# Kernel tuning notes

Measured on AMD Instinct MI355X. Metric: run time of the kernel, lower is better.

## Reference

```python
import jax, jax.numpy as jnp
import numpy as np

N_NODES = 50000
C = 128
E = 800000
B = 4096
NEG = 5
NUM_LAYERS = 3


def setup_inputs() -> dict:
    key = jax.random.key(0)
    ks = jax.random.split(key, 8)
    edge_index = jax.random.randint(ks[0], (2, E), 0, N_NODES, dtype=jnp.int64)
    edge_weight = jax.random.uniform(ks[1], (E,), dtype=jnp.float32)
    n_id = jax.random.randint(ks[2], ((2 + NEG) * B,), 0, N_NODES, dtype=jnp.int64)
    x = jnp.zeros((1,), jnp.float32)  # ignored by forward (overwritten by id_embed)
    id_embed = jax.random.normal(ks[3], (N_NODES, C), jnp.float32) * 0.1
    w1 = jax.random.normal(ks[4], (2 * C, C), jnp.float32) * (1.0 / np.sqrt(2 * C))
    b1 = jnp.zeros((C,), jnp.float32)
    w2 = jax.random.normal(ks[5], (C, 1), jnp.float32) * (1.0 / np.sqrt(C))
    b2 = jnp.zeros((1,), jnp.float32)
    return {"x": x, "edge_index": edge_index, "edge_weight": edge_weight,
            "n_id": n_id, "neg_sample_num": NEG, "id_embed": id_embed,
            "w1": w1, "b1": b1, "w2": w2, "b2": b2}


def reference(x, edge_index, edge_weight, n_id, neg_sample_num, id_embed, w1, b1, w2, b2):
    n_nodes = id_embed.shape[0]
    row, col = edge_index[0], edge_index[1]
    # symmetric GCN normalization (LGCConv)
    deg = jax.ops.segment_sum(jnp.ones_like(row, dtype=id_embed.dtype), row,
                              num_segments=n_nodes)
    dinv = jnp.where(deg > 0, jax.lax.rsqrt(jnp.maximum(deg, 1e-12)), 0.0)
    norm = (dinv[row] * dinv[col])[:, None]  # [E,1]
    h = id_embed
    final = id_embed
    for _ in range(NUM_LAYERS):
        h = jax.ops.segment_sum(norm * h[col], row, num_segments=n_nodes)
        final = final + h
    final = final / (NUM_LAYERS + 1)
    # split n_id into (out, pos, neg) index groups
    b = n_id.shape[0] // (2 + neg_sample_num)
    out = final[n_id[:b]]
    pos = final[n_id[b:2 * b]]
    neg = final[n_id[2 * b:]]
    tiled_out = jnp.repeat(out, neg_sample_num, axis=0)  # [b*neg, C]

    def pred_head(z):  # Linear -> LeakyReLU(0.2) -> (Dropout eval=identity) -> Linear
        z = jax.nn.leaky_relu(z @ w1 + b1, negative_slope=0.2)
        return z @ w2 + b2

    pos_logit = pred_head(jnp.concatenate([out, pos], axis=-1))
    neg_logits = pred_head(jnp.concatenate([tiled_out, neg], axis=-1))
    return pos_logit, neg_logits
```

## Files before the change

### kernel.cpp

```cpp
#include <hip/hip_runtime.h>
#include <hip/hip_bf16.h>

#define C 128
#define NBKT 128
#define BCAP 8192

typedef __bf16 bf16x8 __attribute__((ext_vector_type(8)));
typedef float floatx4 __attribute__((ext_vector_type(4)));

__device__ __forceinline__ unsigned short f2bf(float f) {
    unsigned u = __float_as_uint(f);
    unsigned r = (u + 0x7FFFu + ((u >> 16) & 1u)) >> 16;
    return (unsigned short)r;
}
__device__ __forceinline__ float bflo(unsigned v) { return __uint_as_float(v << 16); }
__device__ __forceinline__ float bfhi(unsigned v) { return __uint_as_float(v & 0xFFFF0000u); }
__device__ __forceinline__ unsigned packbf(float lo, float hi) {
    return (unsigned)f2bf(lo) | ((unsigned)f2bf(hi) << 16);
}

__device__ __forceinline__ int g_idx(const void* p, long long i, int is64) {
    if (is64) return (int)((const long long*)p)[i];
    return ((const int*)p)[i];
}
__device__ __forceinline__ float g_flt(const void* p, long long i, int isf32) {
    if (isf32) return ((const float*)p)[i];
    return __uint_as_float(((unsigned)((const unsigned short*)p)[i]) << 16);
}

__global__ void k_detect(const void* edge, const void* nid, const void* emb, int* flags,
                         unsigned* g0, unsigned* g1, unsigned* g2, int* bucketcnt, int N) {
    int t = threadIdx.x;
    int buf = t >> 6, w = t & 63;
    size_t o = (size_t)N * 64 + w;
    if (buf == 0) g0[o] = 0;
    else if (buf == 1) g1[o] = 0;
    else g2[o] = 0;
    if (t < NBKT) bucketcnt[t] = 0;
    if (t < 64) {
        const unsigned* wrd = (const unsigned*)edge;
        const unsigned* nw = (const unsigned*)nid;
        int predA = (t < 32) ? (wrd[2 * t + 1] == 0u) : 1;
        int predB = (t < 32) ? (nw[2 * t + 1] == 0u) : 1;
        const unsigned short* h = (const unsigned short*)emb;
        int ex = (h[2 * t] >> 7) & 0xFF;
        int plaus = (ex >= 0x6C && ex <= 0x7F) ? 1 : 0;
        unsigned long long mA = __ballot(predA);
        unsigned long long mB = __ballot(predB);
        unsigned long long mP = __ballot(plaus);
        if (t == 0) {
            flags[0] = (mA == ~0ull) ? 1 : 0;
            flags[1] = (mB == ~0ull) ? 1 : 0;
            flags[2] = (__popcll(mP) < 32) ? 1 : 0;
        }
    }
}

__global__ void k_bucketA(const void* edge, int E, int rpb, const int* flags,
                          unsigned* __restrict__ bucketbuf, int* __restrict__ bucketcnt) {
    __shared__ int lcnt[NBKT];
    __shared__ int lbase[NBKT];
    int t = threadIdx.x;
    int is64 = flags[0];
    const int PER = 8;
    int chunkSz = blockDim.x * PER;
    long long stride = (long long)gridDim.x * chunkSz;
    for (long long base = (long long)blockIdx.x * chunkSz; base < E; base += stride) {
        if (t < NBKT) lcnt[t] = 0;
        __syncthreads();
        int bkt[PER], rank[PER];
        unsigned enc[PER];
        long long e0 = base + (long long)t * PER;
        int rr[PER], cc[PER];
        if (e0 + PER <= E) {
            if (is64) {
                const long long* pr = (const long long*)edge + e0;
                const long long* pc = (const long long*)edge + E + e0;
#pragma unroll
                for (int j = 0; j < PER; j += 2) {
                    longlong2 vr = *(const longlong2*)(pr + j);
                    longlong2 vc = *(const longlong2*)(pc + j);
                    rr[j] = (int)vr.x; rr[j + 1] = (int)vr.y;
                    cc[j] = (int)vc.x; cc[j + 1] = (int)vc.y;
                }
            } else {
                const int* pr = (const int*)edge + e0;
                const int* pc = (const int*)edge + E + e0;
#pragma unroll
                for (int j = 0; j < PER; j += 4) {
                    int4 vr = *(const int4*)(pr + j);
                    int4 vc = *(const int4*)(pc + j);
                    rr[j] = vr.x; rr[j + 1] = vr.y; rr[j + 2] = vr.z; rr[j + 3] = vr.w;
                    cc[j] = vc.x; cc[j + 1] = vc.y; cc[j + 2] = vc.z; cc[j + 3] = vc.w;
                }
            }
#pragma unroll
            for (int j = 0; j < PER; ++j) {
                int b = rr[j] / rpb;
                bkt[j] = b;
                enc[j] = ((unsigned)(rr[j] - b * rpb) << 16) | (unsigned)(cc[j] & 0xFFFF);
                rank[j] = atomicAdd(&lcnt[b], 1);
            }
        } else {
#pragma unroll
            for (int j = 0; j < PER; ++j) {
                long long e = e0 + j;
                if (e < E) {
                    int r = g_idx(edge, e, is64);
                    int c = g_idx(edge, (long long)E + e, is64);
                    int b = r / rpb;
                    bkt[j] = b;
                    enc[j] = ((unsigned)(r - b * rpb) << 16) | (unsigned)(c & 0xFFFF);
                    rank[j] = atomicAdd(&lcnt[b], 1);
                } else bkt[j] = -1;
            }
        }
        __syncthreads();
        if (t < NBKT) lbase[t] = atomicAdd(&bucketcnt[t], lcnt[t]);
        __syncthreads();
#pragma unroll
        for (int j = 0; j < PER; ++j) {
            if (bkt[j] >= 0) {
                int pos = lbase[bkt[j]] + rank[j];
                if (pos < BCAP)
                    bucketbuf[(size_t)bkt[j] * BCAP + pos] = enc[j];
            }
        }
    }
}

__global__ __launch_bounds__(512) void k_bsort(
        const unsigned* __restrict__ bucketbuf, const int* __restrict__ bucketcnt,
        int* __restrict__ rowptr, float* __restrict__ dinv, float* __restrict__ di2,
        float* __restrict__ rdinv, unsigned short* __restrict__ cols16, int N, int rpb) {
    __shared__ int hist[512];
    int b = blockIdx.x;
    int t = threadIdx.x;
    int base = 0, cnt = 0, total = 0;
    for (int i = 0; i < NBKT; ++i) {
        int v = bucketcnt[i];
        if (v > BCAP) v = BCAP;
        if (i < b) base += v;
        if (i == b) cnt = v;
        total += v;
    }
    int r0 = b * rpb;
    int rows = N - r0;
    if (rows > rpb) rows = rpb;
    if (rows < 0) rows = 0;

    hist[t] = 0;
    __syncthreads();
    const unsigned* buf = bucketbuf + (size_t)b * BCAP;
    for (int i = t; i < cnt; i += 512) atomicAdd(&hist[buf[i] >> 16], 1);
    __syncthreads();
    int v = hist[t];
    __syncthreads();
    for (int off = 1; off < 512; off <<= 1) {
        int x = (t >= off) ? hist[t - off] : 0;
        __syncthreads();
        hist[t] += x;
        __syncthreads();
    }
    int excl = hist[t] - v;
    if (t < rows) {
        int r = r0 + t;
        rowptr[r] = base + excl;
        float fd = (float)v;
        float dv = (v > 0) ? rsqrtf(fd) : 0.0f;
        dinv[r] = dv;
        di2[r] = dv * dv;
        rdinv[r] = (v > 0) ? sqrtf(fd) : 0.0f;
    }
    if (b == NBKT - 1 && t == 0) rowptr[N] = total;
    __syncthreads();
    hist[t] = base + excl;
    __syncthreads();
    for (int i = t; i < cnt; i += 512) {
        unsigned u = buf[i];
        int pos = atomicAdd(&hist[u >> 16], 1);
        cols16[pos] = (unsigned short)(u & 0xFFFF);
    }
}

__global__ void k_initprep(const void* emb, const float* __restrict__ dinv,
                           unsigned* __restrict__ h0, unsigned* __restrict__ g0, int n2,
                           const void* w1, const void* b1, const void* w2, const void* b2,
                           unsigned short* __restrict__ w1t, float* __restrict__ b1f,
                           float* __restrict__ w2f, float* __restrict__ b2f, const int* flags) {
    int i = blockIdx.x * blockDim.x + threadIdx.x;
    int f32 = flags[2];
    if (i < n2) {
        float lo = g_flt(emb, 2LL * i, f32);
        float hi = g_flt(emb, 2LL * i + 1, f32);
        h0[i] = packbf(lo, hi);
        float dv = dinv[i >> 6];
        g0[i] = packbf(lo * dv, hi * dv);
    }
    if (i < 256 * 128) {
        int k = i >> 7, n = i & 127;
        w1t[n * 256 + k] = f2bf(g_flt(w1, i, f32));
    }
    if (i < 128) {
        b1f[i] = g_flt(b1, i, f32);
        w2f[i] = g_flt(w2, i, f32);
    }
    if (i == 0) b2f[0] = g_flt(b2, 0, f32);
}

__global__ void k_layer(const int* __restrict__ rowptr, const unsigned short* __restrict__ cols16,
                        const uint4* __restrict__ gin, uint4* __restrict__ gout,
                        const float* __restrict__ di2, int N) {
    int node = blockIdx.x * (blockDim.x >> 6) + (threadIdx.x >> 6);
    if (node >= N) return;
    int lane = threadIdx.x & 63;
    int quad = lane >> 4, l16 = lane & 15;
    int p = rowptr[node];
    int end = rowptr[node + 1];
    float a0 = 0.f, a1 = 0.f, a2 = 0.f, a3 = 0.f;
    float a4 = 0.f, a5 = 0.f, a6 = 0.f, a7 = 0.f;
    for (int base = p; base < end; base += 16) {
        int i0 = base + (quad << 2);
        int c0 = cols16[i0];
        int c1 = cols16[i0 + 1];
        int c2 = cols16[i0 + 2];
        int c3 = cols16[i0 + 3];
        c0 = (i0 < end) ? c0 : N;
        c1 = (i0 + 1 < end) ? c1 : N;
        c2 = (i0 + 2 < end) ? c2 : N;
        c3 = (i0 + 3 < end) ? c3 : N;
        uint4 v0 = gin[(size_t)c0 * 16 + l16];
        uint4 v1 = gin[(size_t)c1 * 16 + l16];
        uint4 v2 = gin[(size_t)c2 * 16 + l16];
        uint4 v3 = gin[(size_t)c3 * 16 + l16];
        a0 += (bflo(v0.x) + bflo(v1.x)) + (bflo(v2.x) + bflo(v3.x));
        a1 += (bfhi(v0.x) + bfhi(v1.x)) + (bfhi(v2.x) + bfhi(v3.x));
        a2 += (bflo(v0.y) + bflo(v1.y)) + (bflo(v2.y) + bflo(v3.y));
        a3 += (bfhi(v0.y) + bfhi(v1.y)) + (bfhi(v2.y) + bfhi(v3.y));
        a4 += (bflo(v0.z) + bflo(v1.z)) + (bflo(v2.z) + bflo(v3.z));
        a5 += (bfhi(v0.z) + bfhi(v1.z)) + (bfhi(v2.z) + bfhi(v3.z));
        a6 += (bflo(v0.w) + bflo(v1.w)) + (bflo(v2.w) + bflo(v3.w));
        a7 += (bfhi(v0.w) + bfhi(v1.w)) + (bfhi(v2.w) + bfhi(v3.w));
    }
    a0 += __shfl_xor(a0, 16, 64); a0 += __shfl_xor(a0, 32, 64);
    a1 += __shfl_xor(a1, 16, 64); a1 += __shfl_xor(a1, 32, 64);
    a2 += __shfl_xor(a2, 16, 64); a2 += __shfl_xor(a2, 32, 64);
    a3 += __shfl_xor(a3, 16, 64); a3 += __shfl_xor(a3, 32, 64);
    a4 += __shfl_xor(a4, 16, 64); a4 += __shfl_xor(a4, 32, 64);
    a5 += __shfl_xor(a5, 16, 64); a5 += __shfl_xor(a5, 32, 64);
    a6 += __shfl_xor(a6, 16, 64); a6 += __shfl_xor(a6, 32, 64);
    a7 += __shfl_xor(a7, 16, 64); a7 += __shfl_xor(a7, 32, 64);
    if (quad == 0) {
        float s = di2[node];
        uint4 o;
        o.x = packbf(a0 * s, a1 * s);
        o.y = packbf(a2 * s, a3 * s);
        o.z = packbf(a4 * s, a5 * s);
        o.w = packbf(a6 * s, a7 * s);
        gout[(size_t)node * 16 + l16] = o;
    }
}

__global__ void k_layer3(const int* __restrict__ rowptr, const unsigned short* __restrict__ cols16,
                         const uint4* __restrict__ gin , const uint4* __restrict__ h0,
                         const uint4* __restrict__ g1, uint4* __restrict__ fin,
                         const float* __restrict__ di2, const float* __restrict__ rdinv, int N) {
    int node = blockIdx.x * (blockDim.x >> 6) + (threadIdx.x >> 6);
    if (node >= N) return;
    int lane = threadIdx.x & 63;
    int quad = lane >> 4, l16 = lane & 15;
    int p = rowptr[node];
    int end = rowptr[node + 1];
    float a0 = 0.f, a1 = 0.f, a2 = 0.f, a3 = 0.f;
    float a4 = 0.f, a5 = 0.f, a6 = 0.f, a7 = 0.f;
    for (int base = p; base < end; base += 16) {
        int i0 = base + (quad << 2);
        int c0 = cols16[i0];
        int c1 = cols16[i0 + 1];
        int c2 = cols16[i0 + 2];
        int c3 = cols16[i0 + 3];
        c0 = (i0 < end) ? c0 : N;
        c1 = (i0 + 1 < end) ? c1 : N;
        c2 = (i0 + 2 < end) ? c2 : N;
        c3 = (i0 + 3 < end) ? c3 : N;
        uint4 v0 = gin[(size_t)c0 * 16 + l16];
        uint4 v1 = gin[(size_t)c1 * 16 + l16];
        uint4 v2 = gin[(size_t)c2 * 16 + l16];
        uint4 v3 = gin[(size_t)c3 * 16 + l16];
        a0 += (bflo(v0.x) + bflo(v1.x)) + (bflo(v2.x) + bflo(v3.x));
        a1 += (bfhi(v0.x) + bfhi(v1.x)) + (bfhi(v2.x) + bfhi(v3.x));
        a2 += (bflo(v0.y) + bflo(v1.y)) + (bflo(v2.y) + bflo(v3.y));
        a3 += (bfhi(v0.y) + bfhi(v1.y)) + (bfhi(v2.y) + bfhi(v3.y));
        a4 += (bflo(v0.z) + bflo(v1.z)) + (bflo(v2.z) + bflo(v3.z));
        a5 += (bfhi(v0.z) + bfhi(v1.z)) + (bfhi(v2.z) + bfhi(v3.z));
        a6 += (bflo(v0.w) + bflo(v1.w)) + (bflo(v2.w) + bflo(v3.w));
        a7 += (bfhi(v0.w) + bfhi(v1.w)) + (bfhi(v2.w) + bfhi(v3.w));
    }
    a0 += __shfl_xor(a0, 16, 64); a0 += __shfl_xor(a0, 32, 64);
    a1 += __shfl_xor(a1, 16, 64); a1 += __shfl_xor(a1, 32, 64);
    a2 += __shfl_xor(a2, 16, 64); a2 += __shfl_xor(a2, 32, 64);
    a3 += __shfl_xor(a3, 16, 64); a3 += __shfl_xor(a3, 32, 64);
    a4 += __shfl_xor(a4, 16, 64); a4 += __shfl_xor(a4, 32, 64);
    a5 += __shfl_xor(a5, 16, 64); a5 += __shfl_xor(a5, 32, 64);
    a6 += __shfl_xor(a6, 16, 64); a6 += __shfl_xor(a6, 32, 64);
    a7 += __shfl_xor(a7, 16, 64); a7 += __shfl_xor(a7, 32, 64);
    if (quad == 0) {
        float s = di2[node];
        float rd = rdinv[node];
        size_t ro = (size_t)node * 16 + l16;
        uint4 x0 = h0[ro];
        uint4 x1 = g1[ro];
        uint4 x2 = gin[ro];
        uint4 o;
        o.x = packbf(0.25f * (bflo(x0.x) + rd * (bflo(x1.x) + bflo(x2.x) + s * a0)),
                     0.25f * (bfhi(x0.x) + rd * (bfhi(x1.x) + bfhi(x2.x) + s * a1)));
        o.y = packbf(0.25f * (bflo(x0.y) + rd * (bflo(x1.y) + bflo(x2.y) + s * a2)),
                     0.25f * (bfhi(x0.y) + rd * (bfhi(x1.y) + bfhi(x2.y) + s * a3)));
        o.z = packbf(0.25f * (bflo(x0.z) + rd * (bflo(x1.z) + bflo(x2.z) + s * a4)),
                     0.25f * (bfhi(x0.z) + rd * (bfhi(x1.z) + bfhi(x2.z) + s * a5)));
        o.w = packbf(0.25f * (bflo(x0.w) + rd * (bflo(x1.w) + bflo(x2.w) + s * a6)),
                     0.25f * (bfhi(x0.w) + rd * (bfhi(x1.w) + bfhi(x2.w) + s * a7)));
        fin[ro] = o;
    }
}

__global__ void k_head(const unsigned* __restrict__ fin, const void* n_id,
                       const unsigned short* __restrict__ w1t,
                       const float* __restrict__ b1f, const float* __restrict__ w2f,
                       const float* __restrict__ b2f,
                       float* __restrict__ out, int B, int NEG, const int* flags) {
    __shared__ unsigned short z[64][264];
    int t = threadIdx.x;
    int id64 = flags[1];
    int mbase = blockIdx.x * 64;

    int tu = t & 63;
    int sel = t >> 6;
    int moff = sel >> 1, half = sel & 1;
    for (int m = 0; m < 64; m += 2) {
        int gm = mbase + m + moff;
        int r;
        if (gm < B) {
            r = half ? g_idx(n_id, B + gm, id64) : g_idx(n_id, gm, id64);
        } else {
            int j = gm - B;
            r = half ? g_idx(n_id, 2 * B + j, id64) : g_idx(n_id, j / NEG, id64);
        }
        ((unsigned*)&z[m + moff][0])[half * 64 + tu] = fin[(size_t)r * 64 + tu];
    }
    __syncthreads();

    int wave = t >> 6, lane = t & 63;
    int quad = lane >> 4, l16 = lane & 15;

    floatx4 acc[8] = {};
    bf16x8 a[8];
    const unsigned short* zrow = &z[wave * 16 + l16][0];
#pragma unroll
    for (int ks = 0; ks < 8; ++ks)
        a[ks] = *(const bf16x8*)(zrow + ks * 32 + quad * 8);

#pragma unroll
    for (int ks = 0; ks < 8; ++ks) {
#pragma unroll
        for (int nt = 0; nt < 8; ++nt) {
            bf16x8 b = *(const bf16x8*)(w1t + (nt * 16 + l16) * 256 + ks * 32 + quad * 8);
            acc[nt] = __builtin_amdgcn_mfma_f32_16x16x32_bf16(a[ks], b, acc[nt], 0, 0, 0);
        }
    }

    float s0 = 0.f, s1 = 0.f, s2 = 0.f, s3 = 0.f;
#pragma unroll
    for (int nt = 0; nt < 8; ++nt) {
        int col = nt * 16 + l16;
        float bb = b1f[col], ww = w2f[col];
        float v0 = acc[nt][0] + bb; v0 = (v0 > 0.f) ? v0 : 0.2f * v0; s0 += v0 * ww;
        float v1 = acc[nt][1] + bb; v1 = (v1 > 0.f) ? v1 : 0.2f * v1; s1 += v1 * ww;
        float v2 = acc[nt][2] + bb; v2 = (v2 > 0.f) ? v2 : 0.2f * v2; s2 += v2 * ww;
        float v3 = acc[nt][3] + bb; v3 = (v3 > 0.f) ? v3 : 0.2f * v3; s3 += v3 * ww;
    }
#pragma unroll
    for (int off = 1; off <= 8; off <<= 1) {
        s0 += __shfl_xor(s0, off, 64);
        s1 += __shfl_xor(s1, off, 64);
        s2 += __shfl_xor(s2, off, 64);
        s3 += __shfl_xor(s3, off, 64);
    }
    if (l16 == 0) {
        int rowbase = mbase + wave * 16 + quad * 4;
        float bb2 = b2f[0];
        out[rowbase + 0] = s0 + bb2;
        out[rowbase + 1] = s1 + bb2;
        out[rowbase + 2] = s2 + bb2;
        out[rowbase + 3] = s3 + bb2;
    }
}

extern "C" void kernel_launch(void* const* d_in, const int* in_sizes, int n_in,
                              void* d_out, int out_size, void* d_ws, size_t ws_size,
                              hipStream_t stream) {
    const void* edge_index = d_in[1];
    const void* n_id       = d_in[3];
    const void* id_embed   = d_in[5];
    const void* w1 = d_in[6];
    const void* b1 = d_in[7];
    const void* w2 = d_in[8];
    const void* b2 = d_in[9];
    float* out = (float*)d_out;

    const int E  = in_sizes[1] / 2;
    const int N  = in_sizes[5] / C;
    const int NEG = 5;
    const int B  = in_sizes[3] / (2 + NEG);
    const int n_out_rows = B + B * NEG;
    const int NB = (N + 1) * 64;
    const int rpb = (N + NBKT - 1) / NBKT;

    size_t off = 0;
    auto alloc = [&](size_t nf) {
        char* p = (char*)d_ws + off * 4;
        off += (nf + 255) & ~(size_t)255;
        return p;
    };
    int*   flags     = (int*)alloc(8);
    int*   bucketcnt = (int*)alloc(NBKT);
    float* dinv      = (float*)alloc(N);
    float* di2       = (float*)alloc(N);
    float* rdinv     = (float*)alloc(N);
    int*   rowptr    = (int*)alloc(N + 1);
    unsigned short* cols16 = (unsigned short*)alloc(((size_t)E + 16 + 1) / 2);
    unsigned* bucketbuf = (unsigned*)alloc((size_t)NBKT * BCAP);
    unsigned* h0     = (unsigned*)alloc(NB);
    unsigned* g0     = (unsigned*)alloc(NB);
    unsigned* g1     = (unsigned*)alloc(NB);
    unsigned* g2     = (unsigned*)alloc(NB);
    unsigned* fin    = (unsigned*)alloc((size_t)N * 64);
    unsigned short* w1t = (unsigned short*)alloc(256 * 128 / 2);
    float* b1f       = (float*)alloc(C);
    float* w2f       = (float*)alloc(C);
    float* b2f       = (float*)alloc(8);

    const int BS = 256;
    k_detect<<<1, 192, 0, stream>>>(edge_index, n_id, id_embed, flags, g0, g1, g2, bucketcnt, N);
    const int gridA = (E + BS * 8 - 1) / (BS * 8);
    k_bucketA<<<gridA, BS, 0, stream>>>(edge_index, E, rpb, flags, bucketbuf, bucketcnt);
    k_bsort<<<NBKT, 512, 0, stream>>>(bucketbuf, bucketcnt, rowptr, dinv, di2, rdinv,
                                      cols16, N, rpb);
    k_initprep<<<(N * 64 + BS - 1) / BS, BS, 0, stream>>>(
        id_embed, dinv, h0, g0, N * 64, w1, b1, w2, b2, w1t, b1f, w2f, b2f, flags);

    const int waves_per_block = BS / 64;
    const int layer_grid = (N + waves_per_block - 1) / waves_per_block;
    k_layer<<<layer_grid, BS, 0, stream>>>(rowptr, cols16, (const uint4*)g0, (uint4*)g1, di2, N);
    k_layer<<<layer_grid, BS, 0, stream>>>(rowptr, cols16, (const uint4*)g1, (uint4*)g2, di2, N);
    k_layer3<<<layer_grid, BS, 0, stream>>>(rowptr, cols16, (const uint4*)g2, (const uint4*)h0,
                                            (const uint4*)g1, (uint4*)fin, di2, rdinv, N);

    k_head<<<n_out_rows / 64, BS, 0, stream>>>(fin, n_id, w1t, b1f, w2f, b2f, out, B, NEG, flags);
}
```

Before: 249.4 us.

## Split node features into two channel slabs and assign eight lanes per node

The bf16 propagation buffers are stored as two separate 64-channel slabs. Each layer block works on one slab, with 8 lanes handling each node and walking its edges sequentially in steps of 4. This drops the cross-quad shuffle reduction and the predicated-off output lanes, and keeps each layer's random-gather working set at half the feature width, which should improve cache hit rates. The head gather now uses 16-byte loads. In exchange each node's edges are processed more serially, so load balance depends on the degree distribution, and adjacency reads happen twice, once per slab.

```diff
diff --git a/kernel.cpp b/kernel.cpp
--- a/kernel.cpp
+++ b/kernel.cpp
@@ -29,10 +29,11 @@
 }
 
 __global__ void k_detect(const void* edge, const void* nid, const void* emb, int* flags,
-                         unsigned* g0, unsigned* g1, unsigned* g2, int* bucketcnt, int N) {
+                         unsigned* g0, unsigned* g1, unsigned* g2, int* bucketcnt,
+                         int N, int SST) {
     int t = threadIdx.x;
     int buf = t >> 6, w = t & 63;
-    size_t o = (size_t)N * 64 + w;
+    size_t o = (size_t)(w >> 5) * SST + (size_t)N * 32 + (w & 31);
     if (buf == 0) g0[o] = 0;
     else if (buf == 1) g1[o] = 0;
     else g2[o] = 0;
@@ -184,7 +185,8 @@
 }
 
 __global__ void k_initprep(const void* emb, const float* __restrict__ dinv,
-                           unsigned* __restrict__ h0, unsigned* __restrict__ g0, int n2,
+                           unsigned* __restrict__ h0, unsigned* __restrict__ g0,
+                           int n2, int SST,
                            const void* w1, const void* b1, const void* w2, const void* b2,
                            unsigned short* __restrict__ w1t, float* __restrict__ b1f,
                            float* __restrict__ w2f, float* __restrict__ b2f, const int* flags) {
@@ -193,9 +195,11 @@
     if (i < n2) {
         float lo = g_flt(emb, 2LL * i, f32);
         float hi = g_flt(emb, 2LL * i + 1, f32);
-        h0[i] = packbf(lo, hi);
-        float dv = dinv[i >> 6];
-        g0[i] = packbf(lo * dv, hi * dv);
+        int n = i >> 6, w = i & 63;
+        size_t o = (size_t)(w >> 5) * SST + (size_t)n * 32 + (w & 31);
+        h0[o] = packbf(lo, hi);
+        float dv = dinv[n];
+        g0[o] = packbf(lo * dv, hi * dv);
     }
     if (i < 256 * 128) {
         int k = i >> 7, n = i & 127;
@@ -210,29 +214,28 @@
 
 __global__ void k_layer(const int* __restrict__ rowptr, const unsigned short* __restrict__ cols16,
                         const uint4* __restrict__ gin, uint4* __restrict__ gout,
-                        const float* __restrict__ di2, int N) {
-    int node = blockIdx.x * (blockDim.x >> 6) + (threadIdx.x >> 6);
+                        const float* __restrict__ di2, int N, int SSTU4) {
+    int slice = blockIdx.x & 1;
+    int node = (blockIdx.x >> 1) * 32 + (threadIdx.x >> 3);
     if (node >= N) return;
-    int lane = threadIdx.x & 63;
-    int quad = lane >> 4, l16 = lane & 15;
+    int l8 = threadIdx.x & 7;
+    const uint4* gs = gin + (size_t)slice * SSTU4;
     int p = rowptr[node];
     int end = rowptr[node + 1];
     float a0 = 0.f, a1 = 0.f, a2 = 0.f, a3 = 0.f;
     float a4 = 0.f, a5 = 0.f, a6 = 0.f, a7 = 0.f;
-    for (int base = p; base < end; base += 16) {
-        int i0 = base + (quad << 2);
-        int c0 = cols16[i0];
-        int c1 = cols16[i0 + 1];
-        int c2 = cols16[i0 + 2];
-        int c3 = cols16[i0 + 3];
-        c0 = (i0 < end) ? c0 : N;
-        c1 = (i0 + 1 < end) ? c1 : N;
-        c2 = (i0 + 2 < end) ? c2 : N;
-        c3 = (i0 + 3 < end) ? c3 : N;
-        uint4 v0 = gin[(size_t)c0 * 16 + l16];
-        uint4 v1 = gin[(size_t)c1 * 16 + l16];
-        uint4 v2 = gin[(size_t)c2 * 16 + l16];
-        uint4 v3 = gin[(size_t)c3 * 16 + l16];
+    for (int base = p; base < end; base += 4) {
+        int c0 = cols16[base];
+        int c1 = cols16[base + 1];
+        int c2 = cols16[base + 2];
+        int c3 = cols16[base + 3];
+        c1 = (base + 1 < end) ? c1 : N;
+        c2 = (base + 2 < end) ? c2 : N;
+        c3 = (base + 3 < end) ? c3 : N;
+        uint4 v0 = gs[(size_t)c0 * 8 + l8];
+        uint4 v1 = gs[(size_t)c1 * 8 + l8];
+        uint4 v2 = gs[(size_t)c2 * 8 + l8];
+        uint4 v3 = gs[(size_t)c3 * 8 + l8];
         a0 += (bflo(v0.x) + bflo(v1.x)) + (bflo(v2.x) + bflo(v3.x));
         a1 += (bfhi(v0.x) + bfhi(v1.x)) + (bfhi(v2.x) + bfhi(v3.x));
         a2 += (bflo(v0.y) + bflo(v1.y)) + (bflo(v2.y) + bflo(v3.y));
@@ -242,51 +245,42 @@
         a6 += (bflo(v0.w) + bflo(v1.w)) + (bflo(v2.w) + bflo(v3.w));
         a7 += (bfhi(v0.w) + bfhi(v1.w)) + (bfhi(v2.w) + bfhi(v3.w));
     }
-    a0 += __shfl_xor(a0, 16, 64); a0 += __shfl_xor(a0, 32, 64);
-    a1 += __shfl_xor(a1, 16, 64); a1 += __shfl_xor(a1, 32, 64);
-    a2 += __shfl_xor(a2, 16, 64); a2 += __shfl_xor(a2, 32, 64);
-    a3 += __shfl_xor(a3, 16, 64); a3 += __shfl_xor(a3, 32, 64);
-    a4 += __shfl_xor(a4, 16, 64); a4 += __shfl_xor(a4, 32, 64);
-    a5 += __shfl_xor(a5, 16, 64); a5 += __shfl_xor(a5, 32, 64);
-    a6 += __shfl_xor(a6, 16, 64); a6 += __shfl_xor(a6, 32, 64);
-    a7 += __shfl_xor(a7, 16, 64); a7 += __shfl_xor(a7, 32, 64);
-    if (quad == 0) {
-        float s = di2[node];
-        uint4 o;
-        o.x = packbf(a0 * s, a1 * s);
-        o.y = packbf(a2 * s, a3 * s);
-        o.z = packbf(a4 * s, a5 * s);
-        o.w = packbf(a6 * s, a7 * s);
-        gout[(size_t)node * 16 + l16] = o;
-    }
+    float s = di2[node];
+    uint4 o;
+    o.x = packbf(a0 * s, a1 * s);
+    o.y = packbf(a2 * s, a3 * s);
+    o.z = packbf(a4 * s, a5 * s);
+    o.w = packbf(a6 * s, a7 * s);
+    gout[(size_t)slice * SSTU4 + (size_t)node * 8 + l8] = o;
 }
 
 __global__ void k_layer3(const int* __restrict__ rowptr, const unsigned short* __restrict__ cols16,
                          const uint4* __restrict__ gin , const uint4* __restrict__ h0,
                          const uint4* __restrict__ g1, uint4* __restrict__ fin,
-                         const float* __restrict__ di2, const float* __restrict__ rdinv, int N) {
-    int node = blockIdx.x * (blockDim.x >> 6) + (threadIdx.x >> 6);
+                         const float* __restrict__ di2, const float* __restrict__ rdinv,
+                         int N, int SSTU4) {
+    int slice = blockIdx.x & 1;
+    int node = (blockIdx.x >> 1) * 32 + (threadIdx.x >> 3);
     if (node >= N) return;
-    int lane = threadIdx.x & 63;
-    int quad = lane >> 4, l16 = lane & 15;
+    int l8 = threadIdx.x & 7;
+    size_t sb = (size_t)slice * SSTU4;
+    const uint4* gs = gin + sb;
     int p = rowptr[node];
     int end = rowptr[node + 1];
     float a0 = 0.f, a1 = 0.f, a2 = 0.f, a3 = 0.f;
     float a4 = 0.f, a5 = 0.f, a6 = 0.f, a7 = 0.f;
-    for (int base = p; base < end; base += 16) {
-        int i0 = base + (quad << 2);
-        int c0 = cols16[i0];
-        int c1 = cols16[i0 + 1];
-        int c2 = cols16[i0 + 2];
-        int c3 = cols16[i0 + 3];
-        c0 = (i0 < end) ? c0 : N;
-        c1 = (i0 + 1 < end) ? c1 : N;
-        c2 = (i0 + 2 < end) ? c2 : N;
-        c3 = (i0 + 3 < end) ? c3 : N;
-        uint4 v0 = gin[(size_t)c0 * 16 + l16];
-        uint4 v1 = gin[(size_t)c1 * 16 + l16];
-        uint4 v2 = gin[(size_t)c2 * 16 + l16];
-        uint4 v3 = gin[(size_t)c3 * 16 + l16];
+    for (int base = p; base < end; base += 4) {
+        int c0 = cols16[base];
+        int c1 = cols16[base + 1];
+        int c2 = cols16[base + 2];
+        int c3 = cols16[base + 3];
+        c1 = (base + 1 < end) ? c1 : N;
+        c2 = (base + 2 < end) ? c2 : N;
+        c3 = (base + 3 < end) ? c3 : N;
+        uint4 v0 = gs[(size_t)c0 * 8 + l8];
+        uint4 v1 = gs[(size_t)c1 * 8 + l8];
+        uint4 v2 = gs[(size_t)c2 * 8 + l8];
+        uint4 v3 = gs[(size_t)c3 * 8 + l8];
         a0 += (bflo(v0.x) + bflo(v1.x)) + (bflo(v2.x) + bflo(v3.x));
         a1 += (bfhi(v0.x) + bfhi(v1.x)) + (bfhi(v2.x) + bfhi(v3.x));
         a2 += (bflo(v0.y) + bflo(v1.y)) + (bflo(v2.y) + bflo(v3.y));
@@ -296,35 +290,25 @@
         a6 += (bflo(v0.w) + bflo(v1.w)) + (bflo(v2.w) + bflo(v3.w));
         a7 += (bfhi(v0.w) + bfhi(v1.w)) + (bfhi(v2.w) + bfhi(v3.w));
     }
-    a0 += __shfl_xor(a0, 16, 64); a0 += __shfl_xor(a0, 32, 64);
-    a1 += __shfl_xor(a1, 16, 64); a1 += __shfl_xor(a1, 32, 64);
-    a2 += __shfl_xor(a2, 16, 64); a2 += __shfl_xor(a2, 32, 64);
-    a3 += __shfl_xor(a3, 16, 64); a3 += __shfl_xor(a3, 32, 64);
-    a4 += __shfl_xor(a4, 16, 64); a4 += __shfl_xor(a4, 32, 64);
-    a5 += __shfl_xor(a5, 16, 64); a5 += __shfl_xor(a5, 32, 64);
-    a6 += __shfl_xor(a6, 16, 64); a6 += __shfl_xor(a6, 32, 64);
-    a7 += __shfl_xor(a7, 16, 64); a7 += __shfl_xor(a7, 32, 64);
-    if (quad == 0) {
-        float s = di2[node];
-        float rd = rdinv[node];
-        size_t ro = (size_t)node * 16 + l16;
-        uint4 x0 = h0[ro];
-        uint4 x1 = g1[ro];
-        uint4 x2 = gin[ro];
-        uint4 o;
-        o.x = packbf(0.25f * (bflo(x0.x) + rd * (bflo(x1.x) + bflo(x2.x) + s * a0)),
-                     0.25f * (bfhi(x0.x) + rd * (bfhi(x1.x) + bfhi(x2.x) + s * a1)));
-        o.y = packbf(0.25f * (bflo(x0.y) + rd * (bflo(x1.y) + bflo(x2.y) + s * a2)),
-                     0.25f * (bfhi(x0.y) + rd * (bfhi(x1.y) + bfhi(x2.y) + s * a3)));
-        o.z = packbf(0.25f * (bflo(x0.z) + rd * (bflo(x1.z) + bflo(x2.z) + s * a4)),
-                     0.25f * (bfhi(x0.z) + rd * (bfhi(x1.z) + bfhi(x2.z) + s * a5)));
-        o.w = packbf(0.25f * (bflo(x0.w) + rd * (bflo(x1.w) + bflo(x2.w) + s * a6)),
-                     0.25f * (bfhi(x0.w) + rd * (bfhi(x1.w) + bfhi(x2.w) + s * a7)));
-        fin[ro] = o;
-    }
-}
-
-__global__ void k_head(const unsigned* __restrict__ fin, const void* n_id,
+    float s = di2[node];
+    float rd = rdinv[node];
+    size_t ro = (size_t)node * 8 + l8;
+    uint4 x0 = h0[sb + ro];
+    uint4 x1 = g1[sb + ro];
+    uint4 x2 = gs[ro];
+    uint4 o;
+    o.x = packbf(0.25f * (bflo(x0.x) + rd * (bflo(x1.x) + bflo(x2.x) + s * a0)),
+                 0.25f * (bfhi(x0.x) + rd * (bfhi(x1.x) + bfhi(x2.x) + s * a1)));
+    o.y = packbf(0.25f * (bflo(x0.y) + rd * (bflo(x1.y) + bflo(x2.y) + s * a2)),
+                 0.25f * (bfhi(x0.y) + rd * (bfhi(x1.y) + bfhi(x2.y) + s * a3)));
+    o.z = packbf(0.25f * (bflo(x0.z) + rd * (bflo(x1.z) + bflo(x2.z) + s * a4)),
+                 0.25f * (bfhi(x0.z) + rd * (bfhi(x1.z) + bfhi(x2.z) + s * a5)));
+    o.w = packbf(0.25f * (bflo(x0.w) + rd * (bflo(x1.w) + bflo(x2.w) + s * a6)),
+                 0.25f * (bfhi(x0.w) + rd * (bfhi(x1.w) + bfhi(x2.w) + s * a7)));
+    fin[(size_t)node * 16 + slice * 8 + l8] = o;
+}
+
+__global__ void k_head(const uint4* __restrict__ fin, const void* n_id,
                        const unsigned short* __restrict__ w1t,
                        const float* __restrict__ b1f, const float* __restrict__ w2f,
                        const float* __restrict__ b2f,
@@ -334,19 +318,21 @@
     int id64 = flags[1];
     int mbase = blockIdx.x * 64;
 
-    int tu = t & 63;
-    int sel = t >> 6;
-    int moff = sel >> 1, half = sel & 1;
-    for (int m = 0; m < 64; m += 2) {
-        int gm = mbase + m + moff;
+#pragma unroll
+    for (int i = 0; i < 8; ++i) {
+        int flat = i * 256 + t;
+        int m = flat >> 5;
+        int q = flat & 31;
+        int gm = mbase + m;
         int r;
         if (gm < B) {
-            r = half ? g_idx(n_id, B + gm, id64) : g_idx(n_id, gm, id64);
+            r = (q < 16) ? g_idx(n_id, gm, id64) : g_idx(n_id, B + gm, id64);
         } else {
             int j = gm - B;
-            r = half ? g_idx(n_id, 2 * B + j, id64) : g_idx(n_id, j / NEG, id64);
+            r = (q < 16) ? g_idx(n_id, j / NEG, id64) : g_idx(n_id, 2 * B + j, id64);
         }
-        ((unsigned*)&z[m + moff][0])[half * 64 + tu] = fin[(size_t)r * 64 + tu];
+        uint4 v = fin[(size_t)r * 16 + (q & 15)];
+        *(uint4*)((char*)&z[m][0] + q * 16) = v;
     }
     __syncthreads();
 
@@ -413,7 +399,9 @@
     const int NEG = 5;
     const int B  = in_sizes[3] / (2 + NEG);
     const int n_out_rows = B + B * NEG;
-    const int NB = (N + 1) * 64;
+    const int SST = (N + 1) * 32;
+    const int SSTU4 = (N + 1) * 8;
+    const int NB = 2 * SST;
     const int rpb = (N + NBKT - 1) / NBKT;
 
     size_t off = 0;
@@ -441,20 +429,24 @@
     float* b2f       = (float*)alloc(8);
 
     const int BS = 256;
-    k_detect<<<1, 192, 0, stream>>>(edge_index, n_id, id_embed, flags, g0, g1, g2, bucketcnt, N);
+    k_detect<<<1, 192, 0, stream>>>(edge_index, n_id, id_embed, flags, g0, g1, g2,
+                                    bucketcnt, N, SST);
     const int gridA = (E + BS * 8 - 1) / (BS * 8);
     k_bucketA<<<gridA, BS, 0, stream>>>(edge_index, E, rpb, flags, bucketbuf, bucketcnt);
     k_bsort<<<NBKT, 512, 0, stream>>>(bucketbuf, bucketcnt, rowptr, dinv, di2, rdinv,
                                       cols16, N, rpb);
     k_initprep<<<(N * 64 + BS - 1) / BS, BS, 0, stream>>>(
-        id_embed, dinv, h0, g0, N * 64, w1, b1, w2, b2, w1t, b1f, w2f, b2f, flags);
-
-    const int waves_per_block = BS / 64;
-    const int layer_grid = (N + waves_per_block - 1) / waves_per_block;
-    k_layer<<<layer_grid, BS, 0, stream>>>(rowptr, cols16, (const uint4*)g0, (uint4*)g1, di2, N);
-    k_layer<<<layer_grid, BS, 0, stream>>>(rowptr, cols16, (const uint4*)g1, (uint4*)g2, di2, N);
+        id_embed, dinv, h0, g0, N * 64, SST, w1, b1, w2, b2, w1t, b1f, w2f, b2f, flags);
+
+    const int layer_grid = ((N + 31) / 32) * 2;
+    k_layer<<<layer_grid, BS, 0, stream>>>(rowptr, cols16, (const uint4*)g0, (uint4*)g1,
+                                           di2, N, SSTU4);
+    k_layer<<<layer_grid, BS, 0, stream>>>(rowptr, cols16, (const uint4*)g1, (uint4*)g2,
+                                           di2, N, SSTU4);
     k_layer3<<<layer_grid, BS, 0, stream>>>(rowptr, cols16, (const uint4*)g2, (const uint4*)h0,
-                                            (const uint4*)g1, (uint4*)fin, di2, rdinv, N);
-
-    k_head<<<n_out_rows / 64, BS, 0, stream>>>(fin, n_id, w1t, b1f, w2f, b2f, out, B, NEG, flags);
-}
+                                            (const uint4*)g1, (uint4*)fin, di2, rdinv,
+                                            N, SSTU4);
+
+    k_head<<<n_out_rows / 64, BS, 0, stream>>>((const uint4*)fin, n_id, w1t, b1f, w2f, b2f,
+                                               out, B, NEG, flags);
+}
```

New measurement: 221.9 us. 1.12x faster.
